# Optimization experiments

Measured on AMD Instinct MI355X. Metric: run time of the kernel, lower is better.

The kernel has to match this reference:

```python
import jax, jax.numpy as jnp
import numpy as np

H = W = 512
FX = FY = min(H, W) * 0.8
CX, CY = W / 2.0, H / 2.0
PAD = 2
N_GAUSS = 262144
DXY = jnp.arange(-2, 3)
W5 = jnp.exp(-(DXY[:, None] ** 2 + DXY[None, :] ** 2).astype(jnp.float32) / 2.0)  # (5,5) gaussian window weights


def setup_inputs() -> dict:
    key = jax.random.key(0)
    k1, k2, k3 = jax.random.split(key, 3)
    means = jax.random.normal(k1, (N_GAUSS, 3), dtype=jnp.float32) * 0.5
    sh_coeffs = jax.random.normal(k2, (N_GAUSS, 3, 16), dtype=jnp.float32) * 0.1
    opacities = jax.random.uniform(k3, (N_GAUSS, 1), dtype=jnp.float32) * 0.5 + 0.1
    # camera looking down -z, translated so gaussians project in-frame
    camera_pose = jnp.eye(4, dtype=jnp.float32).at[2, 3].set(5.0)[None]  # (1,4,4)
    pruning_mask = jnp.ones((N_GAUSS,), dtype=bool)
    return {"camera_pose": camera_pose, "means": means, "sh_coeffs": sh_coeffs,
            "opacities": opacities, "pruning_mask": pruning_mask}


def _render(camera_pose, means, sh_coeffs, opacities, pruning_mask):
    N = means.shape[0]
    homo = jnp.concatenate([means, jnp.ones((N, 1), means.dtype)], axis=1)  # (N,4)
    pose_inv = jnp.linalg.inv(camera_pose[0])
    cam = (pose_inv @ homo.T).T[:, :3]  # (N,3) camera-space means
    z = cam[:, 2]
    x2d = cam[:, 0] * FX / z + CX
    y2d = cam[:, 1] * FY / z + CY
    # int() in torch truncates toward zero
    xi = jnp.trunc(x2d).astype(jnp.int32)
    yi = jnp.trunc(y2d).astype(jnp.int32)
    valid = pruning_mask & (xi >= 0) & (xi < W) & (yi >= 0) & (yi < H)
    colors = jax.nn.sigmoid(sh_coeffs[:, :, 0])  # (N,3), view_directions=None path

    # depth sort, farthest (largest z) first, then sequential alpha blend
    order = jnp.argsort(-z)
    xi = jnp.clip(xi[order] + PAD, PAD, W + PAD - 1)
    yi = jnp.clip(yi[order] + PAD, PAD, H + PAD - 1)
    alpha = opacities[order, 0] * valid[order].astype(means.dtype)  # masked-out -> a=0 -> no-op
    col = colors[order]

    img = jnp.zeros((3, H + 2 * PAD, W + 2 * PAD), means.dtype)  # padded: OOB window writes land in pad & are discarded

    def step(img, g):
        x, y, a, c = g
        ys = y + DXY  # (5,)
        xs = x + DXY  # (5,)
        old = img[:, ys[:, None], xs[None, :]]          # (3,5,5)
        aw = a * W5                                      # (5,5)
        new = (1.0 - aw) * old + aw * c[:, None, None]   # alpha blend
        return img.at[:, ys[:, None], xs[None, :]].set(new), None

    img, _ = jax.lax.scan(step, img, (xi, yi, alpha, col))

    batch = camera_pose.shape[0]
    rendered = jnp.zeros((batch, 3, H, W), means.dtype)
    return rendered.at[0].set(img[:, PAD:PAD + H, PAD:PAD + W])


def reference(camera_pose, means, sh_coeffs, opacities, pruning_mask):
    return _render(camera_pose, means, sh_coeffs, opacities, pruning_mask)
```

## Files before the change

kernel.cpp:

```cpp
#include <hip/hip_runtime.h>
#include <hip/hip_fp16.h>
#include <stdint.h>

typedef uint32_t u32;
typedef uint64_t u64;

#define HWD 512
#define NTX 64
#define NTILES 4096
#define SEG 128
#define MAXSEGS 16384

__device__ __forceinline__ u32 packh2(float a, float b){
  __half2 h=__floats2half2_rn(a,b);
  return *reinterpret_cast<u32*>(&h);
}
__device__ __forceinline__ float2 unph2(u32 bits){
  __half2 h=*reinterpret_cast<__half2*>(&bits);
  return __half22float2(h);
}

__global__ void __launch_bounds__(256) prep_kernel(const float* __restrict__ pose,
    const float* __restrict__ means, const float* __restrict__ sh,
    const float* __restrict__ opac, const u32* __restrict__ maskw,
    u32* __restrict__ keys, u32* __restrict__ xy, float4* __restrict__ rec0,
    u32* __restrict__ h0, int N, int SB){
  __shared__ float pinvS[12];
  __shared__ u32 hh[256];
  __shared__ u32 mflag;
  int t=threadIdx.x, blk=blockIdx.x;
  int i=blk*256+t;
  hh[t]=0u;
  if (t<64){
    u32 w=maskw[t];
    bool isf=(w==0x3F800000u);
    bool ishi=((w&0xFFFFFF00u)!=0u)&&!isf;
    u64 bf=__ballot((int)isf), bh=__ballot((int)ishi);
    if (t==0) mflag = bh? 1u : (bf? 2u : 0u);
  }
  if (t==0){
    double a[4][8];
    for(int r=0;r<4;r++)for(int c=0;c<4;c++){a[r][c]=(double)pose[r*4+c];a[r][4+c]=(r==c)?1.0:0.0;}
    for(int c=0;c<4;c++){
      int p=c;double best=fabs(a[c][c]);
      for(int r=c+1;r<4;r++){double v=fabs(a[r][c]);if(v>best){best=v;p=r;}}
      if(p!=c)for(int j=0;j<8;j++){double tt=a[c][j];a[c][j]=a[p][j];a[p][j]=tt;}
      double inv=1.0/a[c][c];
      for(int j=0;j<8;j++)a[c][j]*=inv;
      for(int r=0;r<4;r++)if(r!=c){double f=a[r][c];for(int j=0;j<8;j++)a[r][j]-=f*a[c][j];}
    }
    for(int r=0;r<3;r++)for(int c=0;c<4;c++) pinvS[r*4+c]=(float)a[r][4+c];
  }
  __syncthreads();
  if (i<N){
    u32 f=mflag;
    bool mk;
    if (f==1u)      mk=(((const unsigned char*)maskw)[i]!=0);
    else if (f==2u) mk=(((const float*)maskw)[i]!=0.0f);
    else            mk=(((const int*)maskw)[i]!=0);
    float x=means[3*i], y=means[3*i+1], z=means[3*i+2];
    float cx=pinvS[0]*x+pinvS[1]*y+pinvS[2]*z+pinvS[3];
    float cy=pinvS[4]*x+pinvS[5]*y+pinvS[6]*z+pinvS[7];
    float cz=pinvS[8]*x+pinvS[9]*y+pinvS[10]*z+pinvS[11];
    float x2d=(cx*409.6f)/cz; x2d=x2d+256.0f;
    float y2d=(cy*409.6f)/cz; y2d=y2d+256.0f;
    bool okx=(x2d>-1.0f)&&(x2d<512.0f);
    bool oky=(y2d>-1.0f)&&(y2d<512.0f);
    bool valid=mk&&okx&&oky;
    int xi=(int)x2d, yi=(int)y2d;
    float alpha= valid? opac[i]:0.0f;
    u32 pk= valid? ((u32)xi|((u32)yi<<16)) : 0xFFFFFFFFu;
    float c0=1.0f/(1.0f+expf(-sh[48*i]));
    float c1=1.0f/(1.0f+expf(-sh[48*i+16]));
    float c2=1.0f/(1.0f+expf(-sh[48*i+32]));
    u32 u=__float_as_uint(cz);
    u32 ou=u^(((u>>31)!=0u)?0xFFFFFFFFu:0x80000000u);
    u32 key=~ou;
    keys[i]=key;
    xy[i]=pk;
    rec0[i]=make_float4(__uint_as_float(pk), c0, c1, __uint_as_float(packh2(c2,alpha)));
    atomicAdd(&hh[key&255u],1u);
  }
  __syncthreads();
  h0[t*SB+blk]=hh[t];
}

__global__ void __launch_bounds__(256) scan1_kernel(const u32* __restrict__ in, u32* __restrict__ out,
                             u32* __restrict__ bsum, int len){
  __shared__ u32 s[256];
  int t=threadIdx.x, blk=blockIdx.x;
  int base=blk*1024 + t*4;
  u32 v0=(base+0<len)?in[base+0]:0u;
  u32 v1=(base+1<len)?in[base+1]:0u;
  u32 v2=(base+2<len)?in[base+2]:0u;
  u32 v3=(base+3<len)?in[base+3]:0u;
  s[t]=v0+v1+v2+v3; __syncthreads();
  for (int off=1;off<256;off<<=1){ u32 x=(t>=off)?s[t-off]:0u; __syncthreads(); s[t]+=x; __syncthreads(); }
  if (t==255) bsum[blk]=s[255];
  u32 run=(t==0)?0u:s[t-1];
  if (base+0<len) out[base+0]=run; run+=v0;
  if (base+1<len) out[base+1]=run; run+=v1;
  if (base+2<len) out[base+2]=run; run+=v2;
  if (base+3<len) out[base+3]=run;
}

template<int NBITS>
__global__ void __launch_bounds__(256) hist_kernel(const u32* __restrict__ keys,
    u32* __restrict__ h, int shift, int n, const u32* __restrict__ nptr, int ipb, int B){
  constexpr int BINS=1<<NBITS;
  __shared__ u32 hh[BINS];
  int t=threadIdx.x, blk=blockIdx.x;
  for (int d=t; d<BINS; d+=256) hh[d]=0u;
  if (nptr) n=(int)*nptr;
  __syncthreads();
  int base=blk*ipb;
  for (int k=0;k<ipb;k+=256){
    int i=base+k+t;
    if (i<n) atomicAdd(&hh[(keys[i]>>shift)&(u32)(BINS-1)],1u);
  }
  __syncthreads();
  for (int d=t; d<BINS; d+=256) h[d*B+blk]=hh[d];
}

template<int NBITS, int MODE, int NW>
__global__ void __launch_bounds__(256) scatter_kernel(
    const u32* __restrict__ kin, const u32* __restrict__ pin,
    u32* __restrict__ kout, u32* __restrict__ pout,
    const u32* __restrict__ histS, const u32* __restrict__ bsum,
    const u32* __restrict__ xy, const float4* __restrict__ recSrc,
    u32* __restrict__ rxy, float4* __restrict__ recDst, u32* __restrict__ ct,
    int shift, int n, const u32* __restrict__ nptr, int ipb, int B){
  constexpr int BINS=1<<NBITS;
  constexpr int C=(NW+255)/256;
  __shared__ u32 base[BINS];
  __shared__ unsigned short wdc[4][BINS];
  __shared__ u32 gwin[NW];
  __shared__ u32 gs[256];
  int t=threadIdx.x, w=t>>6, lane=t&63, blk=blockIdx.x;
  if (nptr) n=(int)*nptr;
  u32 loc[C]; u32 acc=0u;
  #pragma unroll
  for (int q=0;q<C;q++){ int idx=t*C+q; loc[q]=acc; if (idx<NW) acc+=bsum[idx]; }
  gs[t]=acc; __syncthreads();
  for (int off=1;off<256;off<<=1){ u32 x=(t>=off)?gs[t-off]:0u; __syncthreads(); gs[t]+=x; __syncthreads(); }
  u32 tp=(t==0)?0u:gs[t-1];
  #pragma unroll
  for (int q=0;q<C;q++){ int idx=t*C+q; if (idx<NW) gwin[idx]=tp+loc[q]; }
  __syncthreads();
  for (int d=t; d<BINS; d+=256){ u32 e=(u32)d*(u32)B+(u32)blk; base[d]=histS[e]+gwin[e>>10]; }
  for (int d=t; d<4*BINS; d+=256) ((unsigned short*)wdc)[d]=0;
  __syncthreads();
  u64 lt=(1ull<<lane)-1ull;
  int nch=ipb>>8;
  for (int c=0;c<nch;c++){
    int i=blk*ipb + c*256 + t;
    bool live=(i<n);
    u32 key=live?kin[i]:0u;
    u32 pay=0u;
    if constexpr (MODE==0){ pay = pin? (live?pin[i]:0u) : (u32)i; }
    else if constexpr (MODE==1){ pay = live?pin[i]:0u; }
    u32 d=(key>>shift)&(u32)(BINS-1);
    u64 m=~0ull;
    #pragma unroll
    for (int b=0;b<NBITS;b++){ u64 bal=__ballot((int)((d>>b)&1u)); m &= ((d>>b)&1u)?bal:~bal; }
    m &= __ballot((int)live);
    u32 rank=(u32)__popcll(m&lt);
    u32 cnt=(u32)__popcll(m);
    if (live && rank==0u) wdc[w][d]=(unsigned short)cnt;
    __syncthreads();
    if (live){
      u32 off=base[d]+rank;
      for (int w2=0;w2<w;w2++) off+=(u32)wdc[w2][d];
      if constexpr (MODE==0){
        kout[off]=key; pout[off]=pay;
      } else if constexpr (MODE==1){
        u32 pk=xy[pay];
        rxy[off]=pk;
        recDst[off]=recSrc[pay];
        u32 c2=0u;
        if (pk!=0xFFFFFFFFu){
          int xi=(int)(pk&0xFFFFu), yi=(int)(pk>>16);
          int tx0=max(xi-2,0)>>3, tx1=min(xi+2,HWD-1)>>3;
          int ty0=max(yi-2,0)>>3, ty1=min(yi+2,HWD-1)>>3;
          c2=(u32)((tx1-tx0+1)*(ty1-ty0+1));
        }
        ct[off]=c2;
      } else if constexpr (MODE==2){
        kout[off]=key;
      } else {
        kout[off]=key;
        recDst[off]=recSrc[key&0x3FFFFu];
      }
    }
    __syncthreads();
    if (c<nch-1){
      for (int d2=t; d2<BINS; d2+=256){
        base[d2]+=(u32)wdc[0][d2]+(u32)wdc[1][d2]+(u32)wdc[2][d2]+(u32)wdc[3][d2];
        wdc[0][d2]=0; wdc[1][d2]=0; wdc[2][d2]=0; wdc[3][d2]=0;
      }
      __syncthreads();
    }
  }
}

__global__ void __launch_bounds__(256) emit_kernel(const u32* __restrict__ rxy,
    const u32* __restrict__ coffs, const u32* __restrict__ bsum, int nW,
    u32* __restrict__ Mptr, u32* __restrict__ entries, int N){
  __shared__ u32 red[256];
  int t=threadIdx.x, blk=blockIdx.x;
  int w0=blk>>2;
  u32 s=0u;
  for (int j=t;j<w0;j+=256) s+=bsum[j];
  red[t]=s; __syncthreads();
  for (int off=128;off>0;off>>=1){ if(t<off) red[t]+=red[t+off]; __syncthreads(); }
  u32 gpre=red[0];
  if (blk==0){
    __syncthreads();
    u32 s2=0u;
    for (int j=t;j<nW;j+=256) s2+=bsum[j];
    red[t]=s2; __syncthreads();
    for (int off=128;off>0;off>>=1){ if(t<off) red[t]+=red[t+off]; __syncthreads(); }
    if (t==0) *Mptr=red[0];
  }
  int p=blk*256+t; if(p>=N) return;
  u32 pk=rxy[p]; if(pk==0xFFFFFFFFu) return;
  int xi=(int)(pk&0xFFFFu), yi=(int)(pk>>16);
  int tx0=max(xi-2,0)>>3, tx1=min(xi+2,HWD-1)>>3;
  int ty0=max(yi-2,0)>>3, ty1=min(yi+2,HWD-1)>>3;
  u32 o=coffs[p]+gpre;
  for (int ty=ty0;ty<=ty1;ty++)
    for (int tx=tx0;tx<=tx1;tx++){
      entries[o]=((u32)(ty*NTX+tx)<<18)|(u32)p;
      o++;
    }
}

__global__ void __launch_bounds__(256) tbound_kernel(const u32* __restrict__ entries,
    const u32* __restrict__ Mptr, u32* __restrict__ tileoff){
  u32 M=*Mptr;
  u32 i=(u32)blockIdx.x*256u+(u32)threadIdx.x;
  if (i>M) return;
  if (i==M){
    int tlast=(M==0u)? -1 : (int)(entries[M-1]>>18);
    for (int tt=tlast+1; tt<=NTILES; tt++) tileoff[tt]=M;
    return;
  }
  int ti=(int)(entries[i]>>18);
  int tp=(i==0u)? -1 : (int)(entries[i-1]>>18);
  for (int tt=tp+1; tt<=ti; tt++) tileoff[tt]=i;
}

__global__ void __launch_bounds__(256) segscan_kernel(const u32* __restrict__ tileoff,
    u32* __restrict__ segF, u32* __restrict__ segP){
  __shared__ u32 sA[256], sB[256];
  int t=threadIdx.x;
  u32 pF[16], pP[16];
  u32 aF=0u, aP=0u;
  #pragma unroll
  for (int k=0;k<16;k++){
    int tile=t*16+k;
    u32 cnt=tileoff[tile+1]-tileoff[tile];
    pF[k]=aF; aF+=(cnt>>7);
    pP[k]=aP; aP+=((cnt&127u)?1u:0u);
  }
  sA[t]=aF; sB[t]=aP; __syncthreads();
  for (int off=1;off<256;off<<=1){
    u32 xa=(t>=off)?sA[t-off]:0u, xb=(t>=off)?sB[t-off]:0u;
    __syncthreads();
    sA[t]+=xa; sB[t]+=xb;
    __syncthreads();
  }
  u32 b1=(t==0)?0u:sA[t-1], b2=(t==0)?0u:sB[t-1];
  #pragma unroll
  for (int k=0;k<16;k++){
    int tile=t*16+k;
    segF[tile]=b1+pF[k];
    segP[tile]=b2+pP[k];
  }
  if (t==255){ segF[NTILES]=sA[255]; segP[NTILES]=sB[255]; }
}

__global__ void __launch_bounds__(256) renderseg_kernel(const u32* __restrict__ segF,
    const u32* __restrict__ segP, const u32* __restrict__ tileoff,
    const float4* __restrict__ recT, float4* __restrict__ pt){
  __shared__ float2 sxy[4][64];
  __shared__ float4 sc[4][64];
  int t=threadIdx.x, w=t>>6, lane=t&63;
  u32 F=segF[NTILES], P=segP[NTILES];
  u32 k=(u32)blockIdx.x*4u+(u32)w;
  if (k>=F+P) return;
  bool full=(k<F);
  u32 kk= full? k : (k-F);
  const u32* sg= full? segF : segP;
  int lo=0, hi=NTILES-1;
  while (lo<hi){ int mid=(lo+hi+1)>>1; if (sg[mid]<=kk) lo=mid; else hi=mid-1; }
  int tile=lo;
  u32 st=tileoff[tile], en=tileoff[tile+1];
  int s0, s1;
  if (full){ s0=(int)st+(int)(kk-sg[lo])*SEG; s1=s0+SEG; }
  else     { s0=(int)st+(int)((en-st)&~(u32)(SEG-1)); s1=(int)en; }
  float pxf=(float)((tile&(NTX-1))*8+(lane&7));
  float pyf=(float)((tile>>6)*8+(lane>>3));
  float T=1.0f, cr=0.0f, cg=0.0f, cb=0.0f;
  for (int base=s0;base<s1;base+=64){
    int i=base+lane;
    if (i<s1){
      float4 R=recT[i];
      u32 pk=__float_as_uint(R.x);
      sxy[w][lane]=make_float2((float)(pk&0xFFFFu),(float)(pk>>16));
      float2 ca=unph2(__float_as_uint(R.w));
      sc[w][lane]=make_float4(R.y,R.z,ca.x,log2f(ca.y));
    }
    __builtin_amdgcn_wave_barrier();
    int cnt=min(64,s1-base);
    if (cnt==64){
      float Ta=1.0f, ra=0.0f, ga=0.0f, ba=0.0f;
      float Tb=1.0f, rb=0.0f, gb=0.0f, bb=0.0f;
      #pragma unroll 4
      for (int j=0;j<32;j++){
        {
          float2 XY=sxy[w][j]; float4 Cc=sc[w][j];
          float dx=pxf-XY.x, dy=pyf-XY.y;
          float r2=fmaf(dx,dx,dy*dy);
          float aw=exp2f(fmaf(-0.72134752f,r2,Cc.w));
          aw=(r2<=8.0f)?aw:0.0f;
          float om=1.0f-aw;
          Ta*=om;
          ra=fmaf(om,ra,aw*Cc.x);
          ga=fmaf(om,ga,aw*Cc.y);
          ba=fmaf(om,ba,aw*Cc.z);
        }
        {
          float2 XY=sxy[w][j+32]; float4 Cc=sc[w][j+32];
          float dx=pxf-XY.x, dy=pyf-XY.y;
          float r2=fmaf(dx,dx,dy*dy);
          float aw=exp2f(fmaf(-0.72134752f,r2,Cc.w));
          aw=(r2<=8.0f)?aw:0.0f;
          float om=1.0f-aw;
          Tb*=om;
          rb=fmaf(om,rb,aw*Cc.x);
          gb=fmaf(om,gb,aw*Cc.y);
          bb=fmaf(om,bb,aw*Cc.z);
        }
      }
      cr=fmaf(Tb,fmaf(Ta,cr,ra),rb);
      cg=fmaf(Tb,fmaf(Ta,cg,ga),gb);
      cb=fmaf(Tb,fmaf(Ta,cb,ba),bb);
      T*=Ta*Tb;
    } else {
      for (int j=0;j<cnt;j++){
        float2 XY=sxy[w][j]; float4 Cc=sc[w][j];
        float dx=pxf-XY.x, dy=pyf-XY.y;
        float r2=fmaf(dx,dx,dy*dy);
        float aw=exp2f(fmaf(-0.72134752f,r2,Cc.w));
        aw=(r2<=8.0f)?aw:0.0f;
        float om=1.0f-aw;
        T*=om;
        cr=fmaf(om,cr,aw*Cc.x);
        cg=fmaf(om,cg,aw*Cc.y);
        cb=fmaf(om,cb,aw*Cc.z);
      }
    }
    __builtin_amdgcn_wave_barrier();
  }
  pt[k*64u+(u32)lane]=make_float4(T,cr,cg,cb);
}

__global__ void __launch_bounds__(64) combine_kernel(const u32* __restrict__ segF,
    const u32* __restrict__ segP, const u32* __restrict__ tileoff,
    const float4* __restrict__ pt, float* __restrict__ out){
  int tile=blockIdx.x, lane=threadIdx.x;
  u32 F=segF[NTILES];
  u32 a=segF[tile], b=segF[tile+1];
  u32 cnt=tileoff[tile+1]-tileoff[tile];
  float cr=0.0f,cg=0.0f,cb=0.0f;
  for (u32 s=a;s<b;s++){
    float4 Pp=pt[s*64u+(u32)lane];
    cr=Pp.x*cr+Pp.y; cg=Pp.x*cg+Pp.z; cb=Pp.x*cb+Pp.w;
  }
  if (cnt&(u32)(SEG-1)){
    float4 Pp=pt[(F+segP[tile])*64u+(u32)lane];
    cr=Pp.x*cr+Pp.y; cg=Pp.x*cg+Pp.z; cb=Pp.x*cb+Pp.w;
  }
  int px=(tile&(NTX-1))*8+(lane&7), py=(tile/NTX)*8+(lane>>3);
  int o=py*HWD+px;
  out[o]=cr; out[HWD*HWD+o]=cg; out[2*HWD*HWD+o]=cb;
}

extern "C" void kernel_launch(void* const* d_in, const int* in_sizes, int n_in,
                              void* d_out, int out_size, void* d_ws, size_t ws_size,
                              hipStream_t stream){
  const float* pose=(const float*)d_in[0];
  const float* means=(const float*)d_in[1];
  const float* sh=(const float*)d_in[2];
  const float* opac=(const float*)d_in[3];
  const u32* maskw=(const u32*)d_in[4];
  int N=in_sizes[4];
  if (N<=0) return;
  (void)n_in; (void)out_size; (void)ws_size;

  int SB=(N+255)/256;
  const int BT=512;
  int ipbT=(4*N)/BT;

  char* ws=(char*)d_ws; size_t off=0;
  auto alloc=[&](size_t b)->void*{ void* p=(void*)(ws+off); off=(off+b+255)&~(size_t)255; return p; };
  u32* keysA=(u32*)alloc(4ull*N);
  u32* keysB=(u32*)alloc(4ull*N);
  u32* idxA =(u32*)alloc(4ull*N);
  u32* idxB =(u32*)alloc(4ull*N);
  u32* xy   =(u32*)alloc(4ull*N);
  float4* rec0=(float4*)alloc(16ull*N);
  u32* rxy  =(u32*)alloc(4ull*N);
  float4* rec=(float4*)alloc(16ull*N);
  u32* ct   =(u32*)alloc(4ull*N);
  u32* eRaw =(u32*)alloc(4ull*4*N);
  u32* eS   =(u32*)alloc(4ull*4*N);
  float4* recT=(float4*)alloc(16ull*4*N);
  u32* h0=(u32*)alloc(1024ull*SB);
  u32* h1=(u32*)alloc(1024ull*SB);
  u32* h2=(u32*)alloc(1024ull*SB);
  u32* hA=(u32*)alloc(4ull*64*BT);
  u32* hB=(u32*)alloc(4ull*64*BT);
  u32* tileoff=(u32*)alloc(4ull*(NTILES+1));
  u32* segF=(u32*)alloc(4ull*(NTILES+1));
  u32* segP=(u32*)alloc(4ull*(NTILES+1));
  u32* bsum=(u32*)alloc(4ull*4096);
  u32* Mptr=(u32*)alloc(256);
  float4* pt=(float4*)alloc(16ull*64*MAXSEGS);

  prep_kernel<<<SB,256,0,stream>>>(pose,means,sh,opac,maskw,keysA,xy,rec0,h0,N,SB);

  int hlen=256*SB, sbh=(hlen+1023)/1024;
  scan1_kernel<<<sbh,256,0,stream>>>(h0,h0,bsum,hlen);
  scatter_kernel<8,0,256><<<SB,256,0,stream>>>(keysA,nullptr,keysB,idxB,h0,bsum,
      nullptr,nullptr,nullptr,nullptr,nullptr, 0, N,nullptr,256,SB);
  hist_kernel<8><<<SB,256,0,stream>>>(keysB,h1,8,N,nullptr,256,SB);
  scan1_kernel<<<sbh,256,0,stream>>>(h1,h1,bsum,hlen);
  scatter_kernel<8,0,256><<<SB,256,0,stream>>>(keysB,idxB,keysA,idxA,h1,bsum,
      nullptr,nullptr,nullptr,nullptr,nullptr, 8, N,nullptr,256,SB);
  hist_kernel<8><<<SB,256,0,stream>>>(keysA,h2,16,N,nullptr,256,SB);
  scan1_kernel<<<sbh,256,0,stream>>>(h2,h2,bsum,hlen);
  scatter_kernel<8,1,256><<<SB,256,0,stream>>>(keysA,idxA,nullptr,nullptr,h2,bsum,
      xy,rec0,rxy,rec,ct, 16, N,nullptr,256,SB);

  int sbn=(N+1023)/1024;
  scan1_kernel<<<sbn,256,0,stream>>>(ct,ct,bsum,N);
  emit_kernel<<<SB,256,0,stream>>>(rxy,ct,bsum,sbn,Mptr,eRaw,N);

  hist_kernel<6><<<BT,256,0,stream>>>(eRaw,hA,18,0,Mptr,ipbT,BT);
  int tlen=64*BT, sbt=(tlen+1023)/1024;
  scan1_kernel<<<sbt,256,0,stream>>>(hA,hA,bsum,tlen);
  scatter_kernel<6,2,32><<<BT,256,0,stream>>>(eRaw,nullptr,eS,nullptr,hA,bsum,
      nullptr,nullptr,nullptr,nullptr,nullptr, 18, 0,Mptr,ipbT,BT);
  hist_kernel<6><<<BT,256,0,stream>>>(eS,hB,24,0,Mptr,ipbT,BT);
  scan1_kernel<<<sbt,256,0,stream>>>(hB,hB,bsum,tlen);
  scatter_kernel<6,3,32><<<BT,256,0,stream>>>(eS,nullptr,eRaw,nullptr,hB,bsum,
      nullptr,rec,nullptr,recT,nullptr, 24, 0,Mptr,ipbT,BT);

  tbound_kernel<<<(4*N)/256+1,256,0,stream>>>(eRaw,Mptr,tileoff);
  segscan_kernel<<<1,256,0,stream>>>(tileoff,segF,segP);

  renderseg_kernel<<<MAXSEGS/4,256,0,stream>>>(segF,segP,tileoff,recT,pt);
  combine_kernel<<<NTILES,64,0,stream>>>(segF,segP,tileoff,pt,(float*)d_out);
}
```

Before: 172.0 us.

## Precompute segment descriptors, move log2 of alpha to prep, halve sort scatter grid

The segment scan now writes a per-segment descriptor (start, count, tile), so each render wave reads one entry instead of running a binary search over the segment prefix arrays. log2 of alpha is computed once per gaussian in prep and stored in the packed half, rather than per load in the render loop. The three key-sort scatter passes now launch half as many blocks, each covering two histogram columns of 256 items. The single-block segscan takes on serial descriptor writes, and storing log2(alpha) in fp16 changes rounding, with alpha=0 becoming -inf.

Result: slower. 185.6 us (+7.9%).

```diff
diff --git a/kernel.cpp b/kernel.cpp
--- a/kernel.cpp
+++ b/kernel.cpp
@@ -78,7 +78,7 @@
     u32 key=~ou;
     keys[i]=key;
     xy[i]=pk;
-    rec0[i]=make_float4(__uint_as_float(pk), c0, c1, __uint_as_float(packh2(c2,alpha)));
+    rec0[i]=make_float4(__uint_as_float(pk), c0, c1, __uint_as_float(packh2(c2,log2f(alpha))));
     atomicAdd(&hh[key&255u],1u);
   }
   __syncthreads();
@@ -129,7 +129,7 @@
     const u32* __restrict__ histS, const u32* __restrict__ bsum,
     const u32* __restrict__ xy, const float4* __restrict__ recSrc,
     u32* __restrict__ rxy, float4* __restrict__ recDst, u32* __restrict__ ct,
-    int shift, int n, const u32* __restrict__ nptr, int ipb, int B){
+    int shift, int n, const u32* __restrict__ nptr, int ipb, int B, int sub){
   constexpr int BINS=1<<NBITS;
   constexpr int C=(NW+255)/256;
   __shared__ u32 base[BINS];
@@ -147,7 +147,7 @@
   #pragma unroll
   for (int q=0;q<C;q++){ int idx=t*C+q; if (idx<NW) gwin[idx]=tp+loc[q]; }
   __syncthreads();
-  for (int d=t; d<BINS; d+=256){ u32 e=(u32)d*(u32)B+(u32)blk; base[d]=histS[e]+gwin[e>>10]; }
+  for (int d=t; d<BINS; d+=256){ u32 e=(u32)d*(u32)B+(u32)(blk*sub); base[d]=histS[e]+gwin[e>>10]; }
   for (int d=t; d<4*BINS; d+=256) ((unsigned short*)wdc)[d]=0;
   __syncthreads();
   u64 lt=(1ull<<lane)-1ull;
@@ -251,7 +251,7 @@
 }
 
 __global__ void __launch_bounds__(256) segscan_kernel(const u32* __restrict__ tileoff,
-    u32* __restrict__ segF, u32* __restrict__ segP){
+    u32* __restrict__ segF, u32* __restrict__ segP, uint2* __restrict__ segdesc){
   __shared__ u32 sA[256], sB[256];
   int t=threadIdx.x;
   u32 pF[16], pP[16];
@@ -271,34 +271,39 @@
     __syncthreads();
   }
   u32 b1=(t==0)?0u:sA[t-1], b2=(t==0)?0u:sB[t-1];
+  u32 F=sA[255];
   #pragma unroll
   for (int k=0;k<16;k++){
     int tile=t*16+k;
-    segF[tile]=b1+pF[k];
-    segP[tile]=b2+pP[k];
+    u32 st=tileoff[tile];
+    u32 cnt=tileoff[tile+1]-st;
+    u32 f0=b1+pF[k];
+    u32 nf=cnt>>7;
+    for (u32 j=0;j<nf;j++)
+      segdesc[f0+j]=make_uint2(st+j*(u32)SEG, ((u32)tile<<16)|(u32)SEG);
+    u32 p0=b2+pP[k];
+    if (cnt&127u)
+      segdesc[F+p0]=make_uint2(st+(cnt&~127u), ((u32)tile<<16)|(cnt&127u));
+    segF[tile]=f0;
+    segP[tile]=p0;
   }
   if (t==255){ segF[NTILES]=sA[255]; segP[NTILES]=sB[255]; }
 }
 
 __global__ void __launch_bounds__(256) renderseg_kernel(const u32* __restrict__ segF,
-    const u32* __restrict__ segP, const u32* __restrict__ tileoff,
+    const u32* __restrict__ segP, const uint2* __restrict__ segdesc,
     const float4* __restrict__ recT, float4* __restrict__ pt){
   __shared__ float2 sxy[4][64];
   __shared__ float4 sc[4][64];
   int t=threadIdx.x, w=t>>6, lane=t&63;
-  u32 F=segF[NTILES], P=segP[NTILES];
+  u32 nseg=segF[NTILES]+segP[NTILES];
   u32 k=(u32)blockIdx.x*4u+(u32)w;
-  if (k>=F+P) return;
-  bool full=(k<F);
-  u32 kk= full? k : (k-F);
-  const u32* sg= full? segF : segP;
-  int lo=0, hi=NTILES-1;
-  while (lo<hi){ int mid=(lo+hi+1)>>1; if (sg[mid]<=kk) lo=mid; else hi=mid-1; }
-  int tile=lo;
-  u32 st=tileoff[tile], en=tileoff[tile+1];
-  int s0, s1;
-  if (full){ s0=(int)st+(int)(kk-sg[lo])*SEG; s1=s0+SEG; }
-  else     { s0=(int)st+(int)((en-st)&~(u32)(SEG-1)); s1=(int)en; }
+  if (k>=nseg) return;
+  uint2 D=segdesc[k];
+  int s0=(int)D.x;
+  int cnt0=(int)(D.y&0xFFFFu);
+  int tile=(int)(D.y>>16);
+  int s1=s0+cnt0;
   float pxf=(float)((tile&(NTX-1))*8+(lane&7));
   float pyf=(float)((tile>>6)*8+(lane>>3));
   float T=1.0f, cr=0.0f, cg=0.0f, cb=0.0f;
@@ -309,7 +314,7 @@
       u32 pk=__float_as_uint(R.x);
       sxy[w][lane]=make_float2((float)(pk&0xFFFFu),(float)(pk>>16));
       float2 ca=unph2(__float_as_uint(R.w));
-      sc[w][lane]=make_float4(R.y,R.z,ca.x,log2f(ca.y));
+      sc[w][lane]=make_float4(R.y,R.z,ca.x,ca.y);
     }
     __builtin_amdgcn_wave_barrier();
     int cnt=min(64,s1-base);
@@ -367,19 +372,18 @@
 }
 
 __global__ void __launch_bounds__(64) combine_kernel(const u32* __restrict__ segF,
-    const u32* __restrict__ segP, const u32* __restrict__ tileoff,
-    const float4* __restrict__ pt, float* __restrict__ out){
+    const u32* __restrict__ segP, const float4* __restrict__ pt, float* __restrict__ out){
   int tile=blockIdx.x, lane=threadIdx.x;
   u32 F=segF[NTILES];
   u32 a=segF[tile], b=segF[tile+1];
-  u32 cnt=tileoff[tile+1]-tileoff[tile];
+  u32 pa=segP[tile], pb=segP[tile+1];
   float cr=0.0f,cg=0.0f,cb=0.0f;
   for (u32 s=a;s<b;s++){
     float4 Pp=pt[s*64u+(u32)lane];
     cr=Pp.x*cr+Pp.y; cg=Pp.x*cg+Pp.z; cb=Pp.x*cb+Pp.w;
   }
-  if (cnt&(u32)(SEG-1)){
-    float4 Pp=pt[(F+segP[tile])*64u+(u32)lane];
+  if (pb>pa){
+    float4 Pp=pt[(F+pa)*64u+(u32)lane];
     cr=Pp.x*cr+Pp.y; cg=Pp.x*cg+Pp.z; cb=Pp.x*cb+Pp.w;
   }
   int px=(tile&(NTX-1))*8+(lane&7), py=(tile/NTX)*8+(lane>>3);
@@ -400,6 +404,7 @@
   (void)n_in; (void)out_size; (void)ws_size;
 
   int SB=(N+255)/256;
+  int SBS=SB/2;
   const int BT=512;
   int ipbT=(4*N)/BT;
 
@@ -425,6 +430,7 @@
   u32* tileoff=(u32*)alloc(4ull*(NTILES+1));
   u32* segF=(u32*)alloc(4ull*(NTILES+1));
   u32* segP=(u32*)alloc(4ull*(NTILES+1));
+  uint2* segdesc=(uint2*)alloc(8ull*MAXSEGS);
   u32* bsum=(u32*)alloc(4ull*4096);
   u32* Mptr=(u32*)alloc(256);
   float4* pt=(float4*)alloc(16ull*64*MAXSEGS);
@@ -433,16 +439,16 @@
 
   int hlen=256*SB, sbh=(hlen+1023)/1024;
   scan1_kernel<<<sbh,256,0,stream>>>(h0,h0,bsum,hlen);
-  scatter_kernel<8,0,256><<<SB,256,0,stream>>>(keysA,nullptr,keysB,idxB,h0,bsum,
-      nullptr,nullptr,nullptr,nullptr,nullptr, 0, N,nullptr,256,SB);
+  scatter_kernel<8,0,256><<<SBS,256,0,stream>>>(keysA,nullptr,keysB,idxB,h0,bsum,
+      nullptr,nullptr,nullptr,nullptr,nullptr, 0, N,nullptr,512,SB,2);
   hist_kernel<8><<<SB,256,0,stream>>>(keysB,h1,8,N,nullptr,256,SB);
   scan1_kernel<<<sbh,256,0,stream>>>(h1,h1,bsum,hlen);
-  scatter_kernel<8,0,256><<<SB,256,0,stream>>>(keysB,idxB,keysA,idxA,h1,bsum,
-      nullptr,nullptr,nullptr,nullptr,nullptr, 8, N,nullptr,256,SB);
+  scatter_kernel<8,0,256><<<SBS,256,0,stream>>>(keysB,idxB,keysA,idxA,h1,bsum,
+      nullptr,nullptr,nullptr,nullptr,nullptr, 8, N,nullptr,512,SB,2);
   hist_kernel<8><<<SB,256,0,stream>>>(keysA,h2,16,N,nullptr,256,SB);
   scan1_kernel<<<sbh,256,0,stream>>>(h2,h2,bsum,hlen);
-  scatter_kernel<8,1,256><<<SB,256,0,stream>>>(keysA,idxA,nullptr,nullptr,h2,bsum,
-      xy,rec0,rxy,rec,ct, 16, N,nullptr,256,SB);
+  scatter_kernel<8,1,256><<<SBS,256,0,stream>>>(keysA,idxA,nullptr,nullptr,h2,bsum,
+      xy,rec0,rxy,rec,ct, 16, N,nullptr,512,SB,2);
 
   int sbn=(N+1023)/1024;
   scan1_kernel<<<sbn,256,0,stream>>>(ct,ct,bsum,N);
@@ -452,15 +458,15 @@
   int tlen=64*BT, sbt=(tlen+1023)/1024;
   scan1_kernel<<<sbt,256,0,stream>>>(hA,hA,bsum,tlen);
   scatter_kernel<6,2,32><<<BT,256,0,stream>>>(eRaw,nullptr,eS,nullptr,hA,bsum,
-      nullptr,nullptr,nullptr,nullptr,nullptr, 18, 0,Mptr,ipbT,BT);
+      nullptr,nullptr,nullptr,nullptr,nullptr, 18, 0,Mptr,ipbT,BT,1);
   hist_kernel<6><<<BT,256,0,stream>>>(eS,hB,24,0,Mptr,ipbT,BT);
   scan1_kernel<<<sbt,256,0,stream>>>(hB,hB,bsum,tlen);
   scatter_kernel<6,3,32><<<BT,256,0,stream>>>(eS,nullptr,eRaw,nullptr,hB,bsum,
-      nullptr,rec,nullptr,recT,nullptr, 24, 0,Mptr,ipbT,BT);
+      nullptr,rec,nullptr,recT,nullptr, 24, 0,Mptr,ipbT,BT,1);
 
   tbound_kernel<<<(4*N)/256+1,256,0,stream>>>(eRaw,Mptr,tileoff);
-  segscan_kernel<<<1,256,0,stream>>>(tileoff,segF,segP);
-
-  renderseg_kernel<<<MAXSEGS/4,256,0,stream>>>(segF,segP,tileoff,recT,pt);
-  combine_kernel<<<NTILES,64,0,stream>>>(segF,segP,tileoff,pt,(float*)d_out);
-}
+  segscan_kernel<<<1,256,0,stream>>>(tileoff,segF,segP,segdesc);
+
+  renderseg_kernel<<<MAXSEGS/4,256,0,stream>>>(segF,segP,segdesc,recT,pt);
+  combine_kernel<<<NTILES,64,0,stream>>>(segF,segP,pt,(float*)d_out);
+}
```
